# Kernel tuning notes

Measured on AMD Instinct MI355X. Metric: run time of the kernel, lower is better.

Reference implementation:

```python
import jax, jax.numpy as jnp
import numpy as np

N = 262144   # nodes
E = 1048576  # edges (avg degree 4)
DIN = 64     # input node features
H = 128      # hidden channels
DE = 32      # edge feature dim
EPS = 1e-5


def setup_inputs() -> dict:
    key = jax.random.key(0)
    ks = jax.random.split(key, 12)
    s = 0.05
    return {
        "x": jax.random.normal(ks[0], (N, DIN), jnp.float32),
        "edge_attr": jax.random.normal(ks[1], (E, DE), jnp.float32),
        "W_enter": jax.random.normal(ks[2], (H, DIN), jnp.float32) * s,
        "b_enter": jnp.zeros((H,), jnp.float32),
        "W1": jax.random.normal(ks[3], (H, H + DE), jnp.float32) * s,
        "att_l": jax.random.normal(ks[4], (H,), jnp.float32) * s,
        "att_r": jax.random.normal(ks[5], (H,), jnp.float32) * s,
        "W2": jax.random.normal(ks[6], (H, H), jnp.float32) * s,
        "b_conv": jnp.zeros((H,), jnp.float32),
        "W_ih": jax.random.normal(ks[7], (3 * H, H), jnp.float32) * s,
        "W_hh": jax.random.normal(ks[8], (3 * H, H), jnp.float32) * s,
        "b_ih": jnp.zeros((3 * H,), jnp.float32),
        "b_hh": jnp.zeros((3 * H,), jnp.float32),
        "edge_index": jax.random.randint(ks[9], (2, E), 0, N, jnp.int32),
    }


def _segment_softmax(logits, seg, num_segments):
    m = jax.ops.segment_max(logits, seg, num_segments=num_segments)
    e = jnp.exp(logits - m[seg])
    d = jax.ops.segment_sum(e, seg, num_segments=num_segments)
    return e / d[seg]


def reference(x, edge_attr, W_enter, b_enter, W1, att_l, att_r, W2, b_conv,
              W_ih, W_hh, b_ih, b_hh, edge_index):
    n = x.shape[0]
    src, dst = edge_index[0], edge_index[1]  # x_j = x[src], aggregate to dst

    # lin_enter + leaky_relu
    x = jax.nn.leaky_relu(x @ W_enter.T + b_enter)

    # Edge2dConv message: leaky_relu(lin1([x_j, edge_attr]))
    m = jax.nn.leaky_relu(jnp.concatenate([x[src], edge_attr], axis=-1) @ W1.T)  # [E,H]
    alpha = jax.nn.leaky_relu(m @ att_l + x[dst] @ att_r)  # [E]
    alpha = _segment_softmax(alpha, dst, n)
    msg = (m @ W2.T) * alpha[:, None]
    out = jax.ops.segment_sum(msg, dst, num_segments=n) + b_conv

    # elu, then GRUCell(h_in=out_elu, hidden=x)
    h = jax.nn.elu(out)
    gi = h @ W_ih.T + b_ih
    gh = x @ W_hh.T + b_hh
    ir, iz, inn = jnp.split(gi, 3, axis=-1)
    hr, hz, hn = jnp.split(gh, 3, axis=-1)
    r = jax.nn.sigmoid(ir + hr)
    z = jax.nn.sigmoid(iz + hz)
    ncand = jnp.tanh(inn + r * hn)
    x = jax.nn.relu((1.0 - z) * ncand + z * x)

    # layer_norm (no affine)
    mu = jnp.mean(x, axis=-1, keepdims=True)
    var = jnp.mean(jnp.square(x - mu), axis=-1, keepdims=True)
    return (x - mu) / jnp.sqrt(var + EPS)
```

## Files before the change

### kernel.cpp

```cpp
#include <hip/hip_runtime.h>
#include <stdint.h>

#define HD  128
#define DIN 64
#define DE  32

typedef unsigned int u32; typedef unsigned short u16; typedef unsigned char u8;
typedef short s16x8 __attribute__((ext_vector_type(8)));
typedef float f32x4 __attribute__((ext_vector_type(4)));
typedef float f32x2 __attribute__((ext_vector_type(2)));

#define MFMA16(a,b,c) __builtin_amdgcn_mfma_f32_16x16x32_bf16((a),(b),(c),0,0,0)

__device__ __forceinline__ float lrelu(float x){ return x > 0.f ? x : 0.01f*x; }
__device__ __forceinline__ float sigmoidf_(float x){ return 1.f/(1.f + __expf(-x)); }
__device__ __forceinline__ float tanhf_(float x){
    float t = fminf(fmaxf(x, -15.f), 15.f);
    float e = __expf(2.f*t);
    return (e - 1.f)/(e + 1.f);
}
__device__ __forceinline__ float eluf_(float x){ return x > 0.f ? x : expm1f(x); }

__device__ __forceinline__ u16 f32_to_bf16(float x){
    u32 u = __float_as_uint(x);
    u += 0x7FFFu + ((u >> 16) & 1u);
    return (u16)(u >> 16);
}
__device__ __forceinline__ float bf16lo(u32 u){ return __uint_as_float((u & 0xFFFFu) << 16); }
__device__ __forceinline__ float bf16hi(u32 u){ return __uint_as_float(u & 0xFFFF0000u); }
__device__ __forceinline__ float bf16f(u16 h){ return __uint_as_float(((u32)h) << 16); }
__device__ __forceinline__ u32 pk2(float a, float b){
    return (u32)f32_to_bf16(a) | ((u32)f32_to_bf16(b) << 16);
}
__device__ __forceinline__ u8 hw_f8(float v){
    return (u8)__builtin_amdgcn_cvt_pk_fp8_f32(v, v, 0, false);
}
__device__ __forceinline__ f32x2 hw_f8_dec2(u32 u){
    return __builtin_amdgcn_cvt_pk_f32_fp8((int)u, false);
}
__device__ __forceinline__ f32x2 hw_f8_dec2_hi(u32 u){
    return __builtin_amdgcn_cvt_pk_f32_fp8((int)u, true);
}

__device__ __forceinline__ float wave_max(float v){
    #pragma unroll
    for (int o = 32; o > 0; o >>= 1) v = fmaxf(v, __shfl_xor(v, o, 64));
    return v;
}
__device__ __forceinline__ float wave_sum(float v){
    #pragma unroll
    for (int o = 32; o > 0; o >>= 1) v += __shfl_xor(v, o, 64);
    return v;
}
__device__ __forceinline__ float dot8_bf16(uint4 v, const float* __restrict__ al){
    float d = 0.f;
    d = fmaf(bf16lo(v.x), al[0], d); d = fmaf(bf16hi(v.x), al[1], d);
    d = fmaf(bf16lo(v.y), al[2], d); d = fmaf(bf16hi(v.y), al[3], d);
    d = fmaf(bf16lo(v.z), al[4], d); d = fmaf(bf16hi(v.z), al[5], d);
    d = fmaf(bf16lo(v.w), al[6], d); d = fmaf(bf16hi(v.w), al[7], d);
    return d;
}

__global__ void k_prep(const float* __restrict__ W1, const float* __restrict__ W2,
                       const float* __restrict__ Went,
                       const float* __restrict__ Wih, const float* __restrict__ Whh,
                       u16* __restrict__ W1b, u16* __restrict__ W2b,
                       u16* __restrict__ Wentb, u16* __restrict__ Bg)
{
    int i = blockIdx.x*256 + threadIdx.x;
    if (i < 20480){ W1b[i] = f32_to_bf16(W1[i]); return; }
    i -= 20480;
    if (i < 16384){ W2b[i] = f32_to_bf16(W2[i]); return; }
    i -= 16384;
    if (i < 8192){ Wentb[i] = f32_to_bf16(Went[i]); return; }
    i -= 8192;
    if (i < 131072){
        int col = i >> 8, k = i & 255;
        int g = col >> 7, j = col & 127;
        float v;
        if      (g == 0) v = (k < 128) ? Wih[j*128 + k]        : Whh[j*128 + k - 128];
        else if (g == 1) v = (k < 128) ? Wih[(128+j)*128 + k]  : Whh[(128+j)*128 + k - 128];
        else if (g == 2) v = (k < 128) ? Wih[(256+j)*128 + k]  : 0.f;
        else             v = (k < 128) ? 0.f                   : Whh[(256+j)*128 + k - 128];
        Bg[i] = f32_to_bf16(v);
    }
}

__global__ void k_zero2(int* __restrict__ a, int* __restrict__ b, int n){
    int i = blockIdx.x*256 + threadIdx.x;
    if (i < n){ a[i] = 0; b[i] = 0; }
}

__global__ __launch_bounds__(256, 2) void k_enter_mfma(
    const float* __restrict__ x, const u16* __restrict__ Wb, const float* __restrict__ be,
    const float* __restrict__ att_r, u16* __restrict__ Ag, float* __restrict__ r_out, int N)
{
    __shared__ __align__(16) u8 sA[64*144];
    __shared__ __align__(16) u8 sO[64*272];
    int t = threadIdx.x, w = t >> 6, lane = t & 63, l15 = lane & 15, l4 = lane >> 4;
    int tile = blockIdx.x;

    s16x8 bfr[2][2];
    #pragma unroll
    for (int kf = 0; kf < 2; ++kf)
        #pragma unroll
        for (int cf = 0; cf < 2; ++cf)
            bfr[kf][cf] = *(const s16x8*)(Wb + (size_t)(w*32 + cf*16 + l15)*64 + kf*32 + l4*8);

    int el = t >> 2, q = t & 3;
    size_t n = (size_t)tile*64 + el;
    {
        const float4* xs = (const float4*)(x + n*64 + q*16);
        float4 f0 = xs[0], f1 = xs[1], f2 = xs[2], f3 = xs[3];
        uint4 o0, o1;
        o0.x = pk2(f0.x,f0.y); o0.y = pk2(f0.z,f0.w); o0.z = pk2(f1.x,f1.y); o0.w = pk2(f1.z,f1.w);
        o1.x = pk2(f2.x,f2.y); o1.y = pk2(f2.z,f2.w); o1.z = pk2(f3.x,f3.y); o1.w = pk2(f3.z,f3.w);
        *(uint4*)(sA + el*144 + q*32)      = o0;
        *(uint4*)(sA + el*144 + q*32 + 16) = o1;
    }
    __syncthreads();

    f32x4 acc[4][2];
    #pragma unroll
    for (int rf = 0; rf < 4; ++rf){ acc[rf][0] = (f32x4)0.f; acc[rf][1] = (f32x4)0.f; }
    #pragma unroll
    for (int kf = 0; kf < 2; ++kf){
        s16x8 a[4];
        #pragma unroll
        for (int rf = 0; rf < 4; ++rf)
            a[rf] = *(const s16x8*)(sA + (rf*16 + l15)*144 + kf*64 + l4*16);
        #pragma unroll
        for (int rf = 0; rf < 4; ++rf){
            acc[rf][0] = MFMA16(a[rf], bfr[kf][0], acc[rf][0]);
            acc[rf][1] = MFMA16(a[rf], bfr[kf][1], acc[rf][1]);
        }
    }
    float b0 = be[w*32 + l15], b1 = be[w*32 + 16 + l15];
    #pragma unroll
    for (int rf = 0; rf < 4; ++rf)
        #pragma unroll
        for (int r = 0; r < 4; ++r){
            int row = rf*16 + l4*4 + r;
            *(u16*)(sO + row*272 + (w*32 + l15)*2)      = f32_to_bf16(lrelu(acc[rf][0][r] + b0));
            *(u16*)(sO + row*272 + (w*32 + 16 + l15)*2) = f32_to_bf16(lrelu(acc[rf][1][r] + b1));
        }
    __syncthreads();

    float dot = 0.f;
    #pragma unroll
    for (int i = 0; i < 4; ++i){
        uint4 v = *(const uint4*)(sO + el*272 + q*64 + 16*i);
        ((uint4*)Ag)[n*32 + 16 + q*4 + i] = v;
        dot += dot8_bf16(v, att_r + q*32 + 8*i);
    }
    dot += __shfl_xor(dot, 1); dot += __shfl_xor(dot, 2);
    if (q == 0) r_out[n] = dot;
}

__global__ void k_hist(const int* __restrict__ dst, int* __restrict__ deg, int E){
    int e = blockIdx.x*256 + threadIdx.x;
    if (e < E) atomicAdd(&deg[dst[e]], 1);
}
__global__ __launch_bounds__(256) void k_scan_a(
    const int* __restrict__ deg, int* __restrict__ rs, int* __restrict__ btot, int N)
{
    __shared__ int sd[256];
    int b = blockIdx.x, t = threadIdx.x;
    int base = b*1024 + t*4;
    int d0 = deg[base], d1 = deg[base+1], d2 = deg[base+2], d3 = deg[base+3];
    int s = d0 + d1 + d2 + d3;
    sd[t] = s; __syncthreads();
    for (int o = 1; o < 256; o <<= 1){
        int v = (t >= o) ? sd[t-o] : 0;
        __syncthreads();
        sd[t] += v;
        __syncthreads();
    }
    int ex = sd[t] - s;
    rs[base]   = ex;
    rs[base+1] = ex + d0;
    rs[base+2] = ex + d0 + d1;
    rs[base+3] = ex + d0 + d1 + d2;
    if (t == 0) btot[b] = sd[255];
}
__global__ __launch_bounds__(256) void k_scan_b(const int* __restrict__ btot, int* __restrict__ bbase){
    __shared__ int sd[256];
    int t = threadIdx.x;
    int s = btot[t];
    sd[t] = s; __syncthreads();
    for (int o = 1; o < 256; o <<= 1){
        int v = (t >= o) ? sd[t-o] : 0;
        __syncthreads();
        sd[t] += v;
        __syncthreads();
    }
    bbase[t] = sd[t] - s;
}
__global__ void k_scan_c(int* __restrict__ rs, const int* __restrict__ bbase, int N, int E){
    int i = blockIdx.x*256 + threadIdx.x;
    if (i < N) rs[i] += bbase[i >> 10];
    if (i == 0) rs[N] = E;
}
__global__ void k_scatter(const int* __restrict__ dst, const int* __restrict__ rs,
                          int* __restrict__ cnt, int* __restrict__ epos, int E){
    int e = blockIdx.x*256 + threadIdx.x;
    if (e >= E) return;
    int d = dst[e];
    int pos = rs[d] + atomicAdd(&cnt[d], 1);
    epos[e] = pos;
}

__global__ __launch_bounds__(512, 6) void k_edge_mfma(
    const u16* __restrict__ Ag, const float* __restrict__ ea,
    const u16* __restrict__ W1b, const float* __restrict__ att_l,
    const float* __restrict__ r_dst, const int* __restrict__ src, const int* __restrict__ dst,
    const int* __restrict__ epos,
    u8* __restrict__ m, float* __restrict__ alpha, int ntiles, int E)
{
    __shared__ __align__(16) u8 sA[64*336];
    u8* sM = sA;
    int t = threadIdx.x, w = t >> 6, lane = t & 63, l15 = lane & 15, l4 = lane >> 4;

    s16x8 bfr[5];
    #pragma unroll
    for (int kf = 0; kf < 5; ++kf)
        bfr[kf] = *(const s16x8*)(W1b + (size_t)(w*16 + l15)*160 + kf*32 + l4*8);

    int el = t >> 3, q = t & 7;
    int stride = gridDim.x;
    int tile = blockIdx.x;

    uint4 cx0, cx1;
    u32 ce0, ce1;
    {
        int e = tile*64 + el;
        if (tile < ntiles && e < E){
            int sn = src[e];
            const uint4* xs = (const uint4*)Ag + (size_t)sn*32 + 16 + q*2;
            cx0 = xs[0]; cx1 = xs[1];
            float4 f = *(const float4*)(ea + (size_t)e*32 + q*4);
            ce0 = pk2(f.x, f.y); ce1 = pk2(f.z, f.w);
        }
    }

    for (; tile < ntiles; tile += stride){
        int e = tile*64 + el;
        if (e < E){
            uint4* d = (uint4*)(sA + el*336 + q*32);
            d[0] = cx0; d[1] = cx1;
            *(u32*)(sA + el*336 + 256 + q*8)     = ce0;
            *(u32*)(sA + el*336 + 256 + q*8 + 4) = ce1;
        }
        __syncthreads();

        int nt = tile + stride;
        if (nt < ntiles){
            int e2 = nt*64 + el;
            if (e2 < E){
                int sn = src[e2];
                const uint4* xs = (const uint4*)Ag + (size_t)sn*32 + 16 + q*2;
                cx0 = xs[0]; cx1 = xs[1];
                float4 f = *(const float4*)(ea + (size_t)e2*32 + q*4);
                ce0 = pk2(f.x, f.y); ce1 = pk2(f.z, f.w);
            }
        }

        f32x4 acc[4];
        #pragma unroll
        for (int rf = 0; rf < 4; ++rf) acc[rf] = (f32x4)0.f;
        #pragma unroll
        for (int kf = 0; kf < 5; ++kf){
            s16x8 a[4];
            #pragma unroll
            for (int rf = 0; rf < 4; ++rf)
                a[rf] = *(const s16x8*)(sA + (rf*16 + l15)*336 + kf*64 + l4*16);
            #pragma unroll
            for (int rf = 0; rf < 4; ++rf)
                acc[rf] = MFMA16(a[rf], bfr[kf], acc[rf]);
        }
        __syncthreads();

        int col = w*16 + l15;
        #pragma unroll
        for (int rf = 0; rf < 4; ++rf)
            #pragma unroll
            for (int r = 0; r < 4; ++r){
                int row = rf*16 + l4*4 + r;
                sM[row*144 + col] = hw_f8(lrelu(acc[rf][r]));
            }
        __syncthreads();

        if (e < E){
            int p = epos[e];
            uint4 v = *(const uint4*)(sM + el*144 + q*16);
            ((uint4*)m)[(size_t)p*8 + q] = v;
            u32 ws[4] = {v.x, v.y, v.z, v.w};
            float dotv = 0.f;
            #pragma unroll
            for (int i = 0; i < 4; ++i){
                f32x2 fa = hw_f8_dec2(ws[i]);
                f32x2 fb = hw_f8_dec2_hi(ws[i]);
                const float* al = att_l + q*16 + i*4;
                dotv = fmaf(fa.x, al[0], dotv); dotv = fmaf(fa.y, al[1], dotv);
                dotv = fmaf(fb.x, al[2], dotv); dotv = fmaf(fb.y, al[3], dotv);
            }
            dotv += __shfl_xor(dotv, 1); dotv += __shfl_xor(dotv, 2); dotv += __shfl_xor(dotv, 4);
            if (q == 0) alpha[p] = lrelu(dotv + r_dst[dst[e]]);
        }
        __syncthreads();
    }
}

__global__ __launch_bounds__(256) void k_agg(
    const int* __restrict__ rs,
    const float* __restrict__ alpha, const u8* __restrict__ m,
    u16* __restrict__ a_out, int N)
{
    int wid  = (blockIdx.x*256 + threadIdx.x) >> 6;
    int lane = threadIdx.x & 63;
    if (wid >= N) return;
    int s = rs[wid], t = rs[wid+1];
    int deg = t - s;
    float ax = 0.f, ay = 0.f;
    if (deg > 0 && deg <= 64){
        float av = -1e38f;
        if (lane < deg) av = alpha[s + lane];
        float mx = wave_max(av);
        float ev = (lane < deg) ? __expf(av - mx) : 0.f;
        float ssum = wave_sum(ev);
        float wreg = ev / ssum;
        int k = 0;
        for (; k + 2 <= deg; k += 2){
            float w0 = __shfl(wreg, k);
            float w1 = __shfl(wreg, k + 1);
            u32 u0 = *(const u16*)(m + (size_t)(s + k)*HD + 2*lane);
            u32 u1 = *(const u16*)(m + (size_t)(s + k + 1)*HD + 2*lane);
            f32x2 f0 = hw_f8_dec2(u0);
            f32x2 f1 = hw_f8_dec2(u1);
            ax = fmaf(w0, f0.x, ax); ay = fmaf(w0, f0.y, ay);
            ax = fmaf(w1, f1.x, ax); ay = fmaf(w1, f1.y, ay);
        }
        if (k < deg){
            float w0 = __shfl(wreg, k);
            u32 u0 = *(const u16*)(m + (size_t)(s + k)*HD + 2*lane);
            f32x2 f0 = hw_f8_dec2(u0);
            ax = fmaf(w0, f0.x, ax); ay = fmaf(w0, f0.y, ay);
        }
    } else if (deg > 64){
        float mx = -1e38f;
        for (int k = lane; k < deg; k += 64) mx = fmaxf(mx, alpha[s + k]);
        mx = wave_max(mx);
        float ssum = 0.f;
        for (int k = lane; k < deg; k += 64) ssum += __expf(alpha[s + k] - mx);
        ssum = wave_sum(ssum);
        float inv = 1.f / ssum;
        for (int k = 0; k < deg; ++k){
            float wgt = __expf(alpha[s + k] - mx) * inv;
            u32 u0 = *(const u16*)(m + (size_t)(s + k)*HD + 2*lane);
            f32x2 f0 = hw_f8_dec2(u0);
            ax = fmaf(wgt, f0.x, ax);
            ay = fmaf(wgt, f0.y, ay);
        }
    }
    *(u32*)(a_out + (size_t)wid*HD + 2*lane) = pk2(ax, ay);
}

__global__ __launch_bounds__(256, 2) void k_conv2_mfma(
    const u16* __restrict__ a, const u16* __restrict__ W2b, const float* __restrict__ bc,
    u16* __restrict__ Ag, int N)
{
    __shared__ __align__(16) u8 sA[64*272];
    __shared__ __align__(16) u8 sO[64*272];
    int t = threadIdx.x, w = t >> 6, lane = t & 63, l15 = lane & 15, l4 = lane >> 4;
    int tile = blockIdx.x;

    s16x8 bfr[4][2];
    #pragma unroll
    for (int kf = 0; kf < 4; ++kf)
        #pragma unroll
        for (int cf = 0; cf < 2; ++cf)
            bfr[kf][cf] = *(const s16x8*)(W2b + (size_t)(w*32 + cf*16 + l15)*128 + kf*32 + l4*8);

    int el = t >> 2, q = t & 3;
    size_t n = (size_t)tile*64 + el;
    {
        const uint4* as = (const uint4*)(a + n*HD) + q*4;
        uint4 v0 = as[0], v1 = as[1], v2 = as[2], v3 = as[3];
        uint4* d = (uint4*)(sA + el*272 + q*64);
        d[0] = v0; d[1] = v1; d[2] = v2; d[3] = v3;
    }
    __syncthreads();

    f32x4 acc[4][2];
    #pragma unroll
    for (int rf = 0; rf < 4; ++rf){ acc[rf][0] = (f32x4)0.f; acc[rf][1] = (f32x4)0.f; }
    #pragma unroll
    for (int kf = 0; kf < 4; ++kf){
        s16x8 av[4];
        #pragma unroll
        for (int rf = 0; rf < 4; ++rf)
            av[rf] = *(const s16x8*)(sA + (rf*16 + l15)*272 + kf*64 + l4*16);
        #pragma unroll
        for (int rf = 0; rf < 4; ++rf){
            acc[rf][0] = MFMA16(av[rf], bfr[kf][0], acc[rf][0]);
            acc[rf][1] = MFMA16(av[rf], bfr[kf][1], acc[rf][1]);
        }
    }
    float b0 = bc[w*32 + l15], b1 = bc[w*32 + 16 + l15];
    #pragma unroll
    for (int rf = 0; rf < 4; ++rf)
        #pragma unroll
        for (int r = 0; r < 4; ++r){
            int row = rf*16 + l4*4 + r;
            *(u16*)(sO + row*272 + (w*32 + l15)*2)      = f32_to_bf16(eluf_(acc[rf][0][r] + b0));
            *(u16*)(sO + row*272 + (w*32 + 16 + l15)*2) = f32_to_bf16(eluf_(acc[rf][1][r] + b1));
        }
    __syncthreads();
    #pragma unroll
    for (int i = 0; i < 4; ++i){
        uint4 v = *(const uint4*)(sO + el*272 + q*64 + 16*i);
        ((uint4*)Ag)[n*32 + q*4 + i] = v;
    }
}

__global__ __launch_bounds__(512, 3) void k_gru_mfma(
    const u16* __restrict__ Ag, const u16* __restrict__ Bg,
    const float* __restrict__ bih, const float* __restrict__ bhh,
    float* __restrict__ out, int N, int ntiles)
{
    __shared__ __align__(16) u8 sA[32*528];
    __shared__ __align__(16) float sOut[32*132];
    int t = threadIdx.x, w = t >> 6, lane = t & 63, l15 = lane & 15, l4 = lane >> 4;

    s16x8 bfr0[8], bfr1[8], bfr2[4], bfr3[4];
    {
        int jc = w*16 + l15;
        #pragma unroll
        for (int kf = 0; kf < 8; ++kf){
            bfr0[kf] = *(const s16x8*)(Bg + (size_t)(jc)*256       + kf*32 + l4*8);
            bfr1[kf] = *(const s16x8*)(Bg + (size_t)(128 + jc)*256 + kf*32 + l4*8);
        }
        #pragma unroll
        for (int kf = 0; kf < 4; ++kf){
            bfr2[kf] = *(const s16x8*)(Bg + (size_t)(256 + jc)*256 + kf*32 + l4*8);
            bfr3[kf] = *(const s16x8*)(Bg + (size_t)(384 + jc)*256 + (kf+4)*32 + l4*8);
        }
    }
    int j = w*16 + l15;
    float rb = bih[j] + bhh[j];
    float zb = bih[128 + j] + bhh[128 + j];
    float ib = bih[256 + j];
    float hb = bhh[256 + j];

    int el = t >> 4, part = t & 15;
    int stride = gridDim.x;
    int tile = blockIdx.x;
    uint4 pv0, pv1;
    if (tile < ntiles){
        const uint4* gsrc = (const uint4*)Ag + ((size_t)tile*32 + el)*32 + part*2;
        pv0 = gsrc[0]; pv1 = gsrc[1];
    }

    for (; tile < ntiles; tile += stride){
        {
            uint4* d = (uint4*)(sA + el*528 + part*32);
            d[0] = pv0; d[1] = pv1;
        }
        __syncthreads();

        int nt = tile + stride;
        if (nt < ntiles){
            const uint4* gsrc = (const uint4*)Ag + ((size_t)nt*32 + el)*32 + part*2;
            pv0 = gsrc[0]; pv1 = gsrc[1];
        }

        f32x4 acc[2][4];
        #pragma unroll
        for (int rf = 0; rf < 2; ++rf)
            #pragma unroll
            for (int g = 0; g < 4; ++g) acc[rf][g] = (f32x4)0.f;
        #pragma unroll
        for (int kf = 0; kf < 8; ++kf){
            s16x8 a0 = *(const s16x8*)(sA + l15*528 + kf*64 + l4*16);
            s16x8 a1 = *(const s16x8*)(sA + (16 + l15)*528 + kf*64 + l4*16);
            acc[0][0] = MFMA16(a0, bfr0[kf], acc[0][0]);
            acc[1][0] = MFMA16(a1, bfr0[kf], acc[1][0]);
            acc[0][1] = MFMA16(a0, bfr1[kf], acc[0][1]);
            acc[1][1] = MFMA16(a1, bfr1[kf], acc[1][1]);
            if (kf < 4){
                acc[0][2] = MFMA16(a0, bfr2[kf], acc[0][2]);
                acc[1][2] = MFMA16(a1, bfr2[kf], acc[1][2]);
            } else {
                acc[0][3] = MFMA16(a0, bfr3[kf-4], acc[0][3]);
                acc[1][3] = MFMA16(a1, bfr3[kf-4], acc[1][3]);
            }
        }
        #pragma unroll
        for (int rf = 0; rf < 2; ++rf)
            #pragma unroll
            for (int r = 0; r < 4; ++r){
                int rl = rf*16 + l4*4 + r;
                float rr = sigmoidf_(acc[rf][0][r] + rb);
                float zz = sigmoidf_(acc[rf][1][r] + zb);
                float iv = acc[rf][2][r] + ib;
                float hv = acc[rf][3][r] + hb;
                float nc = tanhf_(iv + rr*hv);
                float xej = bf16f(*(const u16*)(sA + rl*528 + 256 + 2*j));
                float v = (1.f - zz)*nc + zz*xej;
                v = fmaxf(v, 0.f);
                sOut[rl*132 + j] = v;
            }
        __syncthreads();
        {
            int row = t >> 4, sub = t & 15;
            const float* rp = sOut + row*132 + sub*8;
            float v0 = rp[0], v1 = rp[1], v2 = rp[2], v3 = rp[3];
            float v4 = rp[4], v5 = rp[5], v6 = rp[6], v7 = rp[7];
            float s1 = v0+v1+v2+v3+v4+v5+v6+v7;
            float s2 = v0*v0+v1*v1+v2*v2+v3*v3+v4*v4+v5*v5+v6*v6+v7*v7;
            #pragma unroll
            for (int o = 1; o < 16; o <<= 1){ s1 += __shfl_xor(s1, o); s2 += __shfl_xor(s2, o); }
            float mu  = s1 * (1.f/128.f);
            float var = s2 * (1.f/128.f) - mu*mu;
            var = fmaxf(var, 0.f);
            float rsd = rsqrtf(var + 1e-5f);
            float* op = out + ((size_t)tile*32 + row)*128 + sub*8;
            float4 o0, o1;
            o0.x = (v0-mu)*rsd; o0.y = (v1-mu)*rsd; o0.z = (v2-mu)*rsd; o0.w = (v3-mu)*rsd;
            o1.x = (v4-mu)*rsd; o1.y = (v5-mu)*rsd; o1.z = (v6-mu)*rsd; o1.w = (v7-mu)*rsd;
            ((float4*)op)[0] = o0; ((float4*)op)[1] = o1;
        }
        __syncthreads();
    }
}

extern "C" void kernel_launch(void* const* d_in, const int* in_sizes, int n_in,
                              void* d_out, int out_size, void* d_ws, size_t ws_size,
                              hipStream_t stream)
{
    const float* x       = (const float*)d_in[0];
    const float* ea      = (const float*)d_in[1];
    const float* W_enter = (const float*)d_in[2];
    const float* b_enter = (const float*)d_in[3];
    const float* W1      = (const float*)d_in[4];
    const float* att_l   = (const float*)d_in[5];
    const float* att_r   = (const float*)d_in[6];
    const float* W2      = (const float*)d_in[7];
    const float* b_conv  = (const float*)d_in[8];
    const float* W_ih    = (const float*)d_in[9];
    const float* W_hh    = (const float*)d_in[10];
    const float* b_ih    = (const float*)d_in[11];
    const float* b_hh    = (const float*)d_in[12];
    const int*   eidx    = (const int*)d_in[13];

    int N = in_sizes[0] / DIN;
    int E = in_sizes[13] / 2;
    const int* src = eidx;
    const int* dst = eidx + E;
    float* out = (float*)d_out;

    size_t off = 0;
    char* base = (char*)d_ws;
    auto alloc = [&](size_t bytes) -> char* {
        char* p = base + off;
        off = (off + bytes + 255) & ~(size_t)255;
        return p;
    };
    u16*   Ag    = (u16*)  alloc((size_t)N*256*2);
    float* r_dst = (float*)alloc((size_t)N*4);
    float* alpha = (float*)alloc((size_t)E*4);
    int*   deg   = (int*)  alloc((size_t)N*4);
    int*   rs    = (int*)  alloc((size_t)(N+1)*4);
    int*   cnt   = (int*)  alloc((size_t)N*4);
    int*   epos  = (int*)  alloc((size_t)E*4);
    int*   btot  = (int*)  alloc(1024);
    int*   bbase = (int*)  alloc(1024);
    u16*   W1b   = (u16*)  alloc(20480*2);
    u16*   W2b   = (u16*)  alloc(16384*2);
    u16*   Wentb = (u16*)  alloc(8192*2);
    u16*   Bg    = (u16*)  alloc(131072*2);
    u8*    mbuf  = (u8*)   alloc((size_t)E*HD);

    u16* a_agg = (u16*)out;

    int ntiles_n64 = N/64, ntiles_e = (E + 63)/64, ntiles_g = N/32;

    k_prep   <<<(176128+255)/256, 256, 0, stream>>>(W1, W2, W_enter, W_ih, W_hh, W1b, W2b, Wentb, Bg);
    k_zero2  <<<(N+255)/256, 256, 0, stream>>>(deg, cnt, N);
    k_enter_mfma<<<ntiles_n64, 256, 0, stream>>>(x, Wentb, b_enter, att_r, Ag, r_dst, N);
    k_hist   <<<(E+255)/256, 256, 0, stream>>>(dst, deg, E);
    k_scan_a <<<N/1024, 256, 0, stream>>>(deg, rs, btot, N);
    k_scan_b <<<1, 256, 0, stream>>>(btot, bbase);
    k_scan_c <<<(N+255)/256, 256, 0, stream>>>(rs, bbase, N, E);
    k_scatter<<<(E+255)/256, 256, 0, stream>>>(dst, rs, cnt, epos, E);
    k_edge_mfma<<<768, 512, 0, stream>>>(Ag, ea, W1b, att_l, r_dst, src, dst, epos,
                                         mbuf, alpha, ntiles_e, E);
    k_agg    <<<(N+3)/4, 256, 0, stream>>>(rs, alpha, mbuf, a_agg, N);
    k_conv2_mfma<<<ntiles_n64, 256, 0, stream>>>(a_agg, W2b, b_conv, Ag, N);
    k_gru_mfma  <<<2048, 512, 0, stream>>>(Ag, Bg, b_ih, b_hh, out, N, ntiles_g);
}
```

Before: 635.6 us.

## Software-pipeline edge kernel epilogue with separate output buffer and fewer barriers

The edge kernel gets its own shared buffer for the quantized message tile instead of reusing the input staging buffer. That lets the previous tile's scatter of m/alpha run while the next tile's loads and MFMAs proceed, and it drops two of the four barriers per tile. epos and r_dst[dst] gathers are also prefetched one tile ahead in registers. Launch bounds are relaxed to 4 blocks/SM and the grid is raised to 1024 blocks, trading more shared memory and registers for fewer synchronizations.

```diff
diff --git a/kernel.cpp b/kernel.cpp
--- a/kernel.cpp
+++ b/kernel.cpp
@@ -210,7 +210,7 @@
     epos[e] = pos;
 }
 
-__global__ __launch_bounds__(512, 6) void k_edge_mfma(
+__global__ __launch_bounds__(512, 4) void k_edge_mfma(
     const u16* __restrict__ Ag, const float* __restrict__ ea,
     const u16* __restrict__ W1b, const float* __restrict__ att_l,
     const float* __restrict__ r_dst, const int* __restrict__ src, const int* __restrict__ dst,
@@ -218,7 +218,7 @@
     u8* __restrict__ m, float* __restrict__ alpha, int ntiles, int E)
 {
     __shared__ __align__(16) u8 sA[64*336];
-    u8* sM = sA;
+    __shared__ __align__(16) u8 sM[64*144];
     int t = threadIdx.x, w = t >> 6, lane = t & 63, l15 = lane & 15, l4 = lane >> 4;
 
     s16x8 bfr[5];
@@ -232,6 +232,8 @@
 
     uint4 cx0, cx1;
     u32 ce0, ce1;
+    int   pe = 0;
+    float rdv = 0.f;
     {
         int e = tile*64 + el;
         if (tile < ntiles && e < E){
@@ -240,8 +242,14 @@
             cx0 = xs[0]; cx1 = xs[1];
             float4 f = *(const float4*)(ea + (size_t)e*32 + q*4);
             ce0 = pk2(f.x, f.y); ce1 = pk2(f.z, f.w);
-        }
-    }
+            pe  = epos[e];
+            rdv = r_dst[dst[e]];
+        }
+    }
+
+    int   ptile = -1;
+    int   pe_prev = 0;
+    float rdv_prev = 0.f;
 
     for (; tile < ntiles; tile += stride){
         int e = tile*64 + el;
@@ -251,7 +259,7 @@
             *(u32*)(sA + el*336 + 256 + q*8)     = ce0;
             *(u32*)(sA + el*336 + 256 + q*8 + 4) = ce1;
         }
-        __syncthreads();
+        int pe_cur = pe; float rdv_cur = rdv;
 
         int nt = tile + stride;
         if (nt < ntiles){
@@ -262,8 +270,31 @@
                 cx0 = xs[0]; cx1 = xs[1];
                 float4 f = *(const float4*)(ea + (size_t)e2*32 + q*4);
                 ce0 = pk2(f.x, f.y); ce1 = pk2(f.z, f.w);
+                pe  = epos[e2];
+                rdv = r_dst[dst[e2]];
             }
         }
+
+        if (ptile >= 0){
+            int ep = ptile*64 + el;
+            if (ep < E){
+                uint4 v = *(const uint4*)(sM + el*144 + q*16);
+                ((uint4*)m)[(size_t)pe_prev*8 + q] = v;
+                u32 ws[4] = {v.x, v.y, v.z, v.w};
+                float dotv = 0.f;
+                #pragma unroll
+                for (int i = 0; i < 4; ++i){
+                    f32x2 fa = hw_f8_dec2(ws[i]);
+                    f32x2 fb = hw_f8_dec2_hi(ws[i]);
+                    const float* al = att_l + q*16 + i*4;
+                    dotv = fmaf(fa.x, al[0], dotv); dotv = fmaf(fa.y, al[1], dotv);
+                    dotv = fmaf(fb.x, al[2], dotv); dotv = fmaf(fb.y, al[3], dotv);
+                }
+                dotv += __shfl_xor(dotv, 1); dotv += __shfl_xor(dotv, 2); dotv += __shfl_xor(dotv, 4);
+                if (q == 0) alpha[pe_prev] = lrelu(dotv + rdv_prev);
+            }
+        }
+        __syncthreads();
 
         f32x4 acc[4];
         #pragma unroll
@@ -278,7 +309,6 @@
             for (int rf = 0; rf < 4; ++rf)
                 acc[rf] = MFMA16(a[rf], bfr[kf], acc[rf]);
         }
-        __syncthreads();
 
         int col = w*16 + l15;
         #pragma unroll
@@ -290,10 +320,14 @@
             }
         __syncthreads();
 
-        if (e < E){
-            int p = epos[e];
+        ptile = tile; pe_prev = pe_cur; rdv_prev = rdv_cur;
+    }
+
+    if (ptile >= 0){
+        int ep = ptile*64 + el;
+        if (ep < E){
             uint4 v = *(const uint4*)(sM + el*144 + q*16);
-            ((uint4*)m)[(size_t)p*8 + q] = v;
+            ((uint4*)m)[(size_t)pe_prev*8 + q] = v;
             u32 ws[4] = {v.x, v.y, v.z, v.w};
             float dotv = 0.f;
             #pragma unroll
@@ -305,9 +339,8 @@
                 dotv = fmaf(fb.x, al[2], dotv); dotv = fmaf(fb.y, al[3], dotv);
             }
             dotv += __shfl_xor(dotv, 1); dotv += __shfl_xor(dotv, 2); dotv += __shfl_xor(dotv, 4);
-            if (q == 0) alpha[p] = lrelu(dotv + r_dst[dst[e]]);
-        }
-        __syncthreads();
+            if (q == 0) alpha[pe_prev] = lrelu(dotv + rdv_prev);
+        }
     }
 }
 
@@ -593,8 +626,8 @@
     k_scan_b <<<1, 256, 0, stream>>>(btot, bbase);
     k_scan_c <<<(N+255)/256, 256, 0, stream>>>(rs, bbase, N, E);
     k_scatter<<<(E+255)/256, 256, 0, stream>>>(dst, rs, cnt, epos, E);
-    k_edge_mfma<<<768, 512, 0, stream>>>(Ag, ea, W1b, att_l, r_dst, src, dst, epos,
-                                         mbuf, alpha, ntiles_e, E);
+    k_edge_mfma<<<1024, 512, 0, stream>>>(Ag, ea, W1b, att_l, r_dst, src, dst, epos,
+                                          mbuf, alpha, ntiles_e, E);
     k_agg    <<<(N+3)/4, 256, 0, stream>>>(rs, alpha, mbuf, a_agg, N);
     k_conv2_mfma<<<ntiles_n64, 256, 0, stream>>>(a_agg, W2b, b_conv, Ag, N);
     k_gru_mfma  <<<2048, 512, 0, stream>>>(Ag, Bg, b_ih, b_hh, out, N, ntiles_g);
```

Measured after the change: 597.2 us. 1.06x faster.
